# Optimization experiments

Hardware: AMD Instinct MI355X
Metric: run time of the kernel (lower is better)

## Reference

```python
import jax, jax.numpy as jnp
import numpy as np

B, D, C = 4096, 4096, 1024


def setup_inputs() -> dict:
    key = jax.random.key(0)
    kx, kw = jax.random.split(key)
    x = jax.random.normal(kx, (B, D), dtype=jnp.float32)
    # kaiming_normal_ with nonlinearity='relu': std = sqrt(2 / fan_in)
    W = jax.random.normal(kw, (C, D), dtype=jnp.float32) * jnp.sqrt(2.0 / D)
    return {"x": x, "W": W}


def reference(x, W):
    # Original: -( (x[:, :, None] - W.T[None, :, :])**2 ).mean(axis=1)
    d = x.shape[1]
    x_sq = jnp.sum(x * x, axis=1, keepdims=True)        # [B, 1]
    w_sq = jnp.sum(W * W, axis=1)[None, :]              # [1, C]
    cross = jnp.einsum('bd,cd->bc', x, W)               # [B, C] tensor-core GEMM
    return -(x_sq - 2.0 * cross + w_sq) / d
```

## Files before the change

kernel.cpp:

```cpp
#include <hip/hip_runtime.h>
#include <hip/hip_bf16.h>


typedef float f32x4 __attribute__((ext_vector_type(4)));
typedef float f32x2 __attribute__((ext_vector_type(2)));
typedef float f32x16 __attribute__((ext_vector_type(16)));
typedef int i32x4 __attribute__((ext_vector_type(4)));
typedef int i32x8 __attribute__((ext_vector_type(8)));

#define BDIM 4096
#define DDIM 4096
#define CDIM 1024
#define TM 128
#define TN 128
#define BK 64
#define NIT (DDIM / BK)
#define SCALE 32.0f
#define INV_SS (1.0f/1024.0f)

#define WAITV(N) asm volatile("s_waitcnt vmcnt(" #N ")" ::: "memory")
#define BAR()    __builtin_amdgcn_s_barrier()

__global__ __launch_bounds__(256) void cvt_rowsq(
    const float* __restrict__ x, const float* __restrict__ W,
    unsigned char* __restrict__ xb, unsigned char* __restrict__ wb,
    float* __restrict__ xsq, float* __restrict__ wsq)
{
    const int lane = threadIdx.x & 63;
    const int row = blockIdx.x * 4 + (threadIdx.x >> 6);

    const float* src;
    unsigned char* dst;
    float* sq;
    if (row < BDIM) {
        src = x + (size_t)row * DDIM;
        dst = xb + (size_t)row * DDIM;
        sq = xsq + row;
    } else {
        int r = row - BDIM;
        src = W + (size_t)r * DDIM;
        dst = wb + (size_t)r * DDIM;
        sq = wsq + r;
    }

    const float4* s4 = (const float4*)src;
    unsigned int* d4 = (unsigned int*)dst;
    float a = 0.f;
    #pragma unroll
    for (int s = 0; s < DDIM / 4 / 64; ++s) {
        float4 f = s4[lane + 64 * s];
        a += f.x * f.x + f.y * f.y + f.z * f.z + f.w * f.w;
        unsigned int p = 0;
        p = __builtin_amdgcn_cvt_pk_fp8_f32(f.x * SCALE, f.y * SCALE, p, false);
        p = __builtin_amdgcn_cvt_pk_fp8_f32(f.z * SCALE, f.w * SCALE, p, true);
        d4[lane + 64 * s] = p;
    }
    #pragma unroll
    for (int off = 32; off > 0; off >>= 1) a += __shfl_down(a, off);
    if (lane == 0) *sq = a;
}


__device__ __forceinline__ i32x8 cat8(i32x4 lo, i32x4 hi) {
    return __builtin_shufflevector(lo, hi, 0, 1, 2, 3, 4, 5, 6, 7);
}

#define MXMFMA(A, Bv, C)                                                  \
    __builtin_amdgcn_mfma_scale_f32_32x32x64_f8f6f4(                      \
        (A), (Bv), (C), 0, 0, 0, 0x7F7F7F7F, 0, 0x7F7F7F7F)

#define GLOAD16(gp, lp)                                                   \
    __builtin_amdgcn_global_load_lds(                                     \
        (const __attribute__((address_space(1))) void*)(gp),              \
        (__attribute__((address_space(3))) void*)(lp), 16, 0, 0)

__global__ __launch_bounds__(256) void gemm_eucl(
    const unsigned char* __restrict__ xb,
    const unsigned char* __restrict__ wb,
    const float* __restrict__ xsq, const float* __restrict__ wsq,
    float* __restrict__ out)
{
    __shared__ unsigned char sm[4 * 16384];

    const int tid = threadIdx.x;
    const int lane = tid & 63;
    const int w = tid >> 6;
    const int wr = w >> 1;
    const int wc = w & 1;
    const int bm = blockIdx.x * TM;
    const int bn = blockIdx.y * TN;

    const int srow = w * 32 + (lane >> 2);
    const int schunk = ((lane & 3) ^ ((lane >> 3) & 3)) * 16;
    const unsigned char* gA0 = xb + (size_t)(bm + srow) * DDIM + schunk;
    const unsigned char* gA1 = gA0 + (size_t)16 * DDIM;
    const unsigned char* gB0 = wb + (size_t)(bn + srow) * DDIM + schunk;
    const unsigned char* gB1 = gB0 + (size_t)16 * DDIM;
    unsigned char* lA0 = sm + w * 2048;
    unsigned char* lA1 = lA0 + 1024;
    unsigned char* lB0 = sm + 8192 + w * 2048;
    unsigned char* lB1 = lB0 + 1024;

#define STAGE(q, t)                                                       \
    do {                                                                  \
        GLOAD16(gA0 + (t) * BK, lA0 + (q) * 16384);                       \
        GLOAD16(gA1 + (t) * BK, lA1 + (q) * 16384);                       \
        GLOAD16(gB0 + (t) * BK, lB0 + (q) * 16384);                       \
        GLOAD16(gB1 + (t) * BK, lB1 + (q) * 16384);                       \
    } while (0)

    const int s_rd = ((lane & 31) >> 1) & 3;
    const int c0s = ((lane >> 5) * 2) ^ s_rd;
    const unsigned char* aR0 = sm + (wr * 64 + (lane & 31)) * 64 + c0s * 16;
    const unsigned char* aR1 = sm + (wr * 64 + (lane & 31)) * 64 + (c0s ^ 1) * 16;
    const unsigned char* bR0 = sm + 8192 + (wc * 64 + (lane & 31)) * 64 + c0s * 16;
    const unsigned char* bR1 = sm + 8192 + (wc * 64 + (lane & 31)) * 64 + (c0s ^ 1) * 16;

    f32x16 acc[4] = {};

#define COMPUTE(qo)                                                       \
    do {                                                                  \
        i32x8 fb0 = cat8(*(const i32x4*)(bR0 + (qo)),                     \
                         *(const i32x4*)(bR1 + (qo)));                    \
        i32x8 fb1 = cat8(*(const i32x4*)(bR0 + (qo) + 2048),              \
                         *(const i32x4*)(bR1 + (qo) + 2048));             \
        i32x8 fa0 = cat8(*(const i32x4*)(aR0 + (qo)),                     \
                         *(const i32x4*)(aR1 + (qo)));                    \
        i32x8 fa1 = cat8(*(const i32x4*)(aR0 + (qo) + 2048),              \
                         *(const i32x4*)(aR1 + (qo) + 2048));             \
        __builtin_amdgcn_s_setprio(1);                                    \
        acc[0] = MXMFMA(fa0, fb0, acc[0]);                                \
        acc[1] = MXMFMA(fa0, fb1, acc[1]);                                \
        acc[2] = MXMFMA(fa1, fb0, acc[2]);                                \
        acc[3] = MXMFMA(fa1, fb1, acc[3]);                                \
        __builtin_amdgcn_s_setprio(0);                                    \
    } while (0)

    STAGE(0, 0);
    STAGE(1, 1);

    #pragma unroll 4
    for (int t = 0; t < NIT - 2; ++t) {
        WAITV(4);
        BAR();
        STAGE((t + 2) & 3, t + 2);
        COMPUTE((t & 3) * 16384);
    }
    WAITV(4); BAR(); COMPUTE(((NIT - 2) & 3) * 16384);
    WAITV(0); BAR(); COMPUTE(((NIT - 1) & 3) * 16384);

    const float c1m = 2.0f * INV_SS / (float)DDIM;
    const float c2 = 1.0f / (float)DDIM;
    const int gn0 = bn + wc * 64 + (lane & 31);
    const int gm_b = bm + wr * 64 + (lane >> 5) * 4;
    const float wv0 = wsq[gn0];
    const float wv1 = wsq[gn0 + 32];
    #pragma unroll
    for (int i = 0; i < 2; ++i)
        #pragma unroll
        for (int g = 0; g < 4; ++g)
            #pragma unroll
            for (int r = 0; r < 4; ++r) {
                const int gm = gm_b + i * 32 + g * 8 + r;
                const float xs = xsq[gm];
                out[(size_t)gm * CDIM + gn0] =
                    acc[i * 2 + 0][g * 4 + r] * c1m - (xs + wv0) * c2;
                out[(size_t)gm * CDIM + gn0 + 32] =
                    acc[i * 2 + 1][g * 4 + r] * c1m - (xs + wv1) * c2;
            }
#undef STAGE
#undef COMPUTE
}

__global__ void fallback_kernel(const float* __restrict__ x, const float* __restrict__ W,
                                float* __restrict__ out)
{
    int c = blockIdx.x * blockDim.x + threadIdx.x;
    int b = blockIdx.y;
    if (c >= CDIM) return;
    const float* xr = x + (size_t)b * DDIM;
    const float* wr = W + (size_t)c * DDIM;
    float xs = 0.f, ws = 0.f, cr = 0.f;
    for (int d = 0; d < DDIM; ++d) {
        float xv = xr[d], wv = wr[d];
        xs += xv * xv; ws += wv * wv; cr += xv * wv;
    }
    out[(size_t)b * CDIM + c] = (2.0f * cr - xs - ws) / (float)DDIM;
}

extern "C" void kernel_launch(void* const* d_in, const int* in_sizes, int n_in,
                              void* d_out, int out_size, void* d_ws, size_t ws_size,
                              hipStream_t stream) {
    const float* x = (const float*)d_in[0];
    const float* W = (const float*)d_in[1];
    float* out = (float*)d_out;

    size_t need = (size_t)(BDIM + CDIM) * DDIM
                + (size_t)(BDIM + CDIM) * sizeof(float);
    if (ws_size < need) {
        fallback_kernel<<<dim3(CDIM / 256, BDIM), 256, 0, stream>>>(x, W, out);
        return;
    }

    unsigned char* xb = (unsigned char*)d_ws;
    unsigned char* wb = xb + (size_t)BDIM * DDIM;
    float* xsq = (float*)(wb + (size_t)CDIM * DDIM);
    float* wsq = xsq + BDIM;

    cvt_rowsq<<<(BDIM + CDIM) / 4, 256, 0, stream>>>(x, W, xb, wb, xsq, wsq);
    gemm_eucl<<<dim3(BDIM / TM, CDIM / TN), 256, 0, stream>>>(xb, wb, xsq, wsq, out);
}
```

Measured before the change: 132.5 us.

## Give each wave private triple-buffered LDS tiles and drop block barriers

After: 136.1 us. +2.7%, slower.

```diff
diff --git a/kernel.cpp b/kernel.cpp
--- a/kernel.cpp
+++ b/kernel.cpp
@@ -19,7 +19,6 @@
 #define INV_SS (1.0f/1024.0f)
 
 #define WAITV(N) asm volatile("s_waitcnt vmcnt(" #N ")" ::: "memory")
-#define BAR()    __builtin_amdgcn_s_barrier()
 
 __global__ __launch_bounds__(256) void cvt_rowsq(
     const float* __restrict__ x, const float* __restrict__ W,
@@ -80,7 +79,7 @@
     const float* __restrict__ xsq, const float* __restrict__ wsq,
     float* __restrict__ out)
 {
-    __shared__ unsigned char sm[4 * 16384];
+    __shared__ unsigned char sm[4 * 3 * 8192];
 
     const int tid = threadIdx.x;
     const int lane = tid & 63;
@@ -90,31 +89,33 @@
     const int bm = blockIdx.x * TM;
     const int bn = blockIdx.y * TN;
 
-    const int srow = w * 32 + (lane >> 2);
+    unsigned char* wbase = sm + w * 24576;
+
+    const int lr = lane >> 2;
     const int schunk = ((lane & 3) ^ ((lane >> 3) & 3)) * 16;
-    const unsigned char* gA0 = xb + (size_t)(bm + srow) * DDIM + schunk;
-    const unsigned char* gA1 = gA0 + (size_t)16 * DDIM;
-    const unsigned char* gB0 = wb + (size_t)(bn + srow) * DDIM + schunk;
-    const unsigned char* gB1 = gB0 + (size_t)16 * DDIM;
-    unsigned char* lA0 = sm + w * 2048;
-    unsigned char* lA1 = lA0 + 1024;
-    unsigned char* lB0 = sm + 8192 + w * 2048;
-    unsigned char* lB1 = lB0 + 1024;
+    const unsigned char* gA[4];
+    const unsigned char* gB[4];
+    #pragma unroll
+    for (int i = 0; i < 4; ++i) {
+        gA[i] = xb + (size_t)(bm + wr * 64 + 16 * i + lr) * DDIM + schunk;
+        gB[i] = wb + (size_t)(bn + wc * 64 + 16 * i + lr) * DDIM + schunk;
+    }
 
 #define STAGE(q, t)                                                       \
     do {                                                                  \
-        GLOAD16(gA0 + (t) * BK, lA0 + (q) * 16384);                       \
-        GLOAD16(gA1 + (t) * BK, lA1 + (q) * 16384);                       \
-        GLOAD16(gB0 + (t) * BK, lB0 + (q) * 16384);                       \
-        GLOAD16(gB1 + (t) * BK, lB1 + (q) * 16384);                       \
+        _Pragma("unroll")                                                 \
+        for (int i = 0; i < 4; ++i) {                                     \
+            GLOAD16(gA[i] + (t) * BK, wbase + (q) * 8192 + i * 1024);     \
+            GLOAD16(gB[i] + (t) * BK, wbase + (q) * 8192 + 4096 + i * 1024); \
+        }                                                                 \
     } while (0)
 
     const int s_rd = ((lane & 31) >> 1) & 3;
     const int c0s = ((lane >> 5) * 2) ^ s_rd;
-    const unsigned char* aR0 = sm + (wr * 64 + (lane & 31)) * 64 + c0s * 16;
-    const unsigned char* aR1 = sm + (wr * 64 + (lane & 31)) * 64 + (c0s ^ 1) * 16;
-    const unsigned char* bR0 = sm + 8192 + (wc * 64 + (lane & 31)) * 64 + c0s * 16;
-    const unsigned char* bR1 = sm + 8192 + (wc * 64 + (lane & 31)) * 64 + (c0s ^ 1) * 16;
+    const unsigned char* aR0 = wbase + (lane & 31) * 64 + c0s * 16;
+    const unsigned char* aR1 = wbase + (lane & 31) * 64 + (c0s ^ 1) * 16;
+    const unsigned char* bR0 = aR0 + 4096;
+    const unsigned char* bR1 = aR1 + 4096;
 
     f32x16 acc[4] = {};
 
@@ -139,15 +140,16 @@
     STAGE(0, 0);
     STAGE(1, 1);
 
-    #pragma unroll 4
-    for (int t = 0; t < NIT - 2; ++t) {
-        WAITV(4);
-        BAR();
-        STAGE((t + 2) & 3, t + 2);
-        COMPUTE((t & 3) * 16384);
-    }
-    WAITV(4); BAR(); COMPUTE(((NIT - 2) & 3) * 16384);
-    WAITV(0); BAR(); COMPUTE(((NIT - 1) & 3) * 16384);
+    #pragma unroll 6
+    for (int t = 0; t < 60; ++t) {
+        WAITV(8);
+        STAGE((t + 2) % 3, t + 2);
+        COMPUTE((t % 3) * 8192);
+    }
+    WAITV(8); STAGE(2, 62); COMPUTE(0 * 8192);
+    WAITV(8); STAGE(0, 63); COMPUTE(1 * 8192);
+    WAITV(8); COMPUTE(2 * 8192);
+    WAITV(0); COMPUTE(0 * 8192);
 
     const float c1m = 2.0f * INV_SS / (float)DDIM;
     const float c2 = 1.0f / (float)DDIM;
```
